# Kernel tuning notes

Measured on AMD Instinct MI355X. Metric: run time of the kernel, lower is better.

## Reference

```python
import jax, jax.numpy as jnp
import numpy as np

RADIUS = 0.2  # ball_query_radius
K = 64        # max_group_size


def _xavier(key, out_c, in_c):
    lim = float(np.sqrt(6.0 / (in_c + out_c)))
    return jax.random.uniform(key, (out_c, in_c), jnp.float32, -lim, lim)


def setup_inputs() -> dict:
    key = jax.random.key(0)
    ks = jax.random.split(key, 9)
    B, N, C_in, C_out = 8, 4096, 64, 256
    h = C_out // 2
    return {
        "points": jax.random.uniform(ks[0], (B, 3, N), jnp.float32),
        "point_features": jax.random.normal(ks[1], (B, C_in, N), jnp.float32),
        # point_point_net: Conv2d(3,C_in,1) -> ReLU -> Conv2d(C_in,C_in,1) -> ReLU -> Conv2d(C_in,h,1)
        "pw1": _xavier(ks[2], C_in, 3), "pb1": jnp.zeros(C_in, jnp.float32),
        "pw2": _xavier(ks[3], C_in, C_in), "pb2": jnp.zeros(C_in, jnp.float32),
        "pw3": _xavier(ks[4], h, C_in), "pb3": jnp.zeros(h, jnp.float32),
        # feature_point_net: Conv2d(C_in,C_in,1) -> ReLU -> Conv2d(C_in,C_in,1) -> ReLU -> Conv2d(C_in,h,1)
        "fw1": _xavier(ks[5], C_in, C_in), "fb1": jnp.zeros(C_in, jnp.float32),
        "fw2": _xavier(ks[6], C_in, C_in), "fb2": jnp.zeros(C_in, jnp.float32),
        "fw3": _xavier(ks[7], h, C_in), "fb3": jnp.zeros(h, jnp.float32),
    }


def _fps(pts, M):
    """Farthest point sampling: pts [N,3] -> M int32 indices (first pick = 0)."""
    N = pts.shape[0]

    def step(carry, _):
        mind, last = carry
        d = jnp.sum((pts - pts[last]) ** 2, axis=-1)
        mind = jnp.minimum(mind, d)
        nxt = jnp.argmax(mind).astype(jnp.int32)
        return (mind, nxt), last

    init = (jnp.full((N,), jnp.inf, pts.dtype), jnp.int32(0))
    _, idx = jax.lax.scan(step, init, None, length=M)
    return idx


def _ball_group(cent, pts):
    """cent [M,3], pts [N,3] -> first K in-radius neighbor indices [M,K] (padded with first hit)."""
    N = pts.shape[0]
    d2 = jnp.sum((cent[:, None, :] - pts[None, :, :]) ** 2, axis=-1)  # [M,N]
    score = jnp.where(d2 <= RADIUS * RADIUS, jnp.arange(N, dtype=jnp.int32), N)
    neg_top, _ = jax.lax.top_k(-score, K)     # K smallest scores = first K in-radius point ids
    sel = -neg_top                            # [M,K]
    sel = jnp.where(sel < N, sel, sel[:, :1]) # pad misses with first valid (centroid itself, dist 0)
    return sel


def _mlp3(x, w1, b1, w2, b2, w3, b3):
    """1x1 Conv2d stack applied along the channel axis; x [B,M,K,C]."""
    h = jax.nn.relu(jnp.einsum('bmkc,oc->bmko', x, w1) + b1)
    h = jax.nn.relu(jnp.einsum('bmkc,oc->bmko', h, w2) + b2)
    return jnp.einsum('bmkc,oc->bmko', h, w3) + b3


def reference(points, point_features, pw1, pb1, pw2, pb2, pw3, pb3,
              fw1, fb1, fw2, fb2, fw3, fb3):
    B, _, N = points.shape
    M = N // 4
    pts = points.transpose(0, 2, 1)            # [B,N,3]
    feats = point_features.transpose(0, 2, 1)  # [B,N,C]

    idx = jax.vmap(lambda p: _fps(p, M))(pts)                 # [B,M]
    cent = jnp.take_along_axis(pts, idx[:, :, None], axis=1)  # [B,M,3]
    sel = jax.vmap(_ball_group)(cent, pts)                    # [B,M,K]

    gpts = jax.vmap(lambda p, s: p[s])(pts, sel)              # [B,M,K,3]
    rel = gpts - cent[:, :, None, :]                          # local coords around centroid
    gfeat = jax.vmap(lambda f, s: f[s])(feats, sel)           # [B,M,K,C]

    p_out = jnp.max(_mlp3(rel, pw1, pb1, pw2, pb2, pw3, pb3), axis=2)    # [B,M,h]
    f_out = jnp.max(_mlp3(gfeat, fw1, fb1, fw2, fb2, fw3, fb3), axis=2)  # [B,M,h]

    centroid_features = jnp.concatenate([f_out, p_out], axis=-1).transpose(0, 2, 1)  # [B,C_out,M]
    centroids = cent.reshape(B, 3, M)  # replicates torch .view(B,3,-1) on the flat [B*M,3] buffer
    return centroids, centroid_features
```

## Files before the change

kernel.cpp:

```cpp
#include <hip/hip_runtime.h>
#include <hip/hip_bf16.h>

#define BB   8
#define NN   4096
#define MM   1024
#define KK   64
#define CIN  64
#define HH   128

#define R2F 0.039999999105930328f

static __device__ __forceinline__ float rnd_bf16(float v) {
    return __bfloat162float(__float2bfloat16(v));
}
static __device__ __forceinline__ unsigned int bf16bits(float v) {
    unsigned int u = __float_as_uint(v);
    return (u + 0x7FFFu + ((u >> 16) & 1u)) >> 16;
}

__global__ __launch_bounds__(256) void fps_featmlp_kernel(
    const float* __restrict__ pts,
    float* __restrict__ centf,
    float* __restrict__ outc,
    const float* __restrict__ feat,
    const float* __restrict__ fw1, const float* __restrict__ fb1,
    const float* __restrict__ fw2, const float* __restrict__ fb2,
    const float* __restrict__ fw3, const float* __restrict__ fb3,
    __hip_bfloat16* __restrict__ fout)
{
    __shared__ float smem[3 * NN];
    __shared__ unsigned long long akey[4];
    const int t = threadIdx.x;

    if (blockIdx.x < BB) {
        const int b = blockIdx.x;
        float* lx = smem;
        float* ly = smem + NN;
        float* lz = smem + 2 * NN;

        const float* px = pts + (size_t)b * 3 * NN;
        float x[16], y[16], z[16], mind[16];
#pragma unroll
        for (int i = 0; i < 16; ++i) {
            int p = t + i * 256;
            x[i] = px[p];
            y[i] = px[NN + p];
            z[i] = px[2 * NN + p];
            lx[p] = x[i]; ly[p] = y[i]; lz[p] = z[i];
            mind[i] = 3.4e38f;
        }
        if (t < 4) akey[t] = 0ULL;
        __syncthreads();

        float bx = lx[0], by = ly[0], bz = lz[0];

        for (int j = 0; j < MM; ++j) {
            if (t == 0) {
                int o = (b * MM + j) * 3;
                centf[o]    = bx; centf[o + 1] = by; centf[o + 2] = bz;
                outc[o]     = rnd_bf16(bx);
                outc[o + 1] = rnd_bf16(by);
                outc[o + 2] = rnd_bf16(bz);
                akey[(j + 2) & 3] = 0ULL;
            }
            float bd = -1.0f; int bi = 0;
#pragma unroll
            for (int i = 0; i < 16; ++i) {
                float dx = x[i] - bx, dy = y[i] - by, dz = z[i] - bz;
                float d = __fadd_rn(__fadd_rn(__fmul_rn(dx, dx), __fmul_rn(dy, dy)),
                                    __fmul_rn(dz, dz));
                float md = fminf(mind[i], d);
                mind[i] = md;
                if (md > bd) { bd = md; bi = t + i * 256; }
            }
            unsigned long long key =
                ((unsigned long long)__float_as_uint(bd) << 32) |
                (unsigned long long)(0xFFFFFFFFu - (unsigned)bi);
            atomicMax(&akey[j & 3], key);
            __syncthreads();
            unsigned long long bk = akey[j & 3];
            int best = (int)(0xFFFFFFFFu - (unsigned)(bk & 0xFFFFFFFFULL));
            bx = lx[best]; by = ly[best]; bz = lz[best];
        }
    } else {
        float* w1 = smem;
        float* w2 = smem + CIN * CIN;
        for (int i = t; i < CIN * CIN; i += 256) { w1[i] = fw1[i]; w2[i] = fw2[i]; }
        __syncthreads();

        const int gid = (blockIdx.x - BB) * 256 + t;
        const int b = gid >> 12, n = gid & (NN - 1);
        const float* fp = feat + (size_t)b * CIN * NN + n;

        float f[CIN];
#pragma unroll
        for (int c = 0; c < CIN; ++c) f[c] = fp[(size_t)c * NN];

        float h1[CIN];
        for (int o = 0; o < CIN; ++o) {
            float acc = fb1[o];
#pragma unroll
            for (int c = 0; c < CIN; ++c) acc = fmaf(f[c], w1[o * CIN + c], acc);
            h1[o] = fmaxf(acc, 0.f);
        }
        float h2[CIN];
        for (int o = 0; o < CIN; ++o) {
            float acc = fb2[o];
#pragma unroll
            for (int c = 0; c < CIN; ++c) acc = fmaf(h1[c], w2[o * CIN + c], acc);
            h2[o] = fmaxf(acc, 0.f);
        }
        __hip_bfloat16* op = fout + (size_t)gid * HH;
        for (int o = 0; o < HH; ++o) {
            float acc = fb3[o];
#pragma unroll
            for (int c = 0; c < CIN; ++c) acc = fmaf(h2[c], fw3[o * CIN + c], acc);
            op[o] = __float2bfloat16(acc);
        }
    }
}

#define H2SU 36
__global__ __launch_bounds__(64) void groupnet_kernel(
    const float* __restrict__ pts,
    const float* __restrict__ centf,
    const __hip_bfloat16* __restrict__ fout,
    const float* __restrict__ pw1, const float* __restrict__ pb1,
    const float* __restrict__ pw2, const float* __restrict__ pb2,
    const float* __restrict__ pw3, const float* __restrict__ pb3,
    float* __restrict__ outf)
{
    __shared__ unsigned int h2s[KK * H2SU];
    __shared__ int sels[KK];

    const int g = blockIdx.x;
    const int b = g >> 10, m = g & (MM - 1);
    const int lane = threadIdx.x;

    const float* pts_b = pts + (size_t)b * 3 * NN;
    const float cx = centf[(size_t)g * 3];
    const float cy = centf[(size_t)g * 3 + 1];
    const float cz = centf[(size_t)g * 3 + 2];

    int cnt = 0, first = 0;
    bool have_first = false;
    float fx[4], fy[4], fz[4];
#pragma unroll
    for (int q = 0; q < 4; ++q) {
        int p = q * 64 + lane;
        fx[q] = pts_b[p]; fy[q] = pts_b[NN + p]; fz[q] = pts_b[2 * NN + p];
    }
    for (int base = 0; base < NN; base += 256) {
#pragma unroll
        for (int q = 0; q < 4; ++q) {
            const int cb = base + q * 64;
            float vx = fx[q], vy = fy[q], vz = fz[q];
            const int pre = cb + 256 + lane;
            if (pre < NN) {
                fx[q] = pts_b[pre]; fy[q] = pts_b[NN + pre]; fz[q] = pts_b[2 * NN + pre];
            }
            float dx = vx - cx, dy = vy - cy, dz = vz - cz;
            float d2 = __fadd_rn(__fadd_rn(__fmul_rn(dx, dx), __fmul_rn(dy, dy)),
                                 __fmul_rn(dz, dz));
            bool in = (d2 <= R2F);
            unsigned long long mask = __ballot(in);
            if (!have_first && mask != 0ULL) {
                first = cb + (int)__builtin_ctzll(mask);
                have_first = true;
            }
            int pos = cnt + (int)__popcll(mask & ((1ULL << lane) - 1ULL));
            if (in && pos < KK) sels[pos] = cb + lane;
            cnt += (int)__popcll(mask);
        }
    }
    if (cnt < KK) {
        for (int q = cnt + lane; q < KK; q += 64) sels[q] = first;
    }
    __syncthreads();

    const int s = sels[lane];
    float* ob = outf + (size_t)b * 256 * MM + m;

    {
        const float x = pts_b[s]          - cx;
        const float y = pts_b[NN + s]     - cy;
        const float z = pts_b[2 * NN + s] - cz;
        float h1[CIN];
#pragma unroll
        for (int o = 0; o < CIN; ++o) {
            float acc = pb1[o];
            acc = fmaf(x, pw1[o * 3 + 0], acc);
            acc = fmaf(y, pw1[o * 3 + 1], acc);
            acc = fmaf(z, pw1[o * 3 + 2], acc);
            h1[o] = fmaxf(acc, 0.f);
        }
        for (int o8 = 0; o8 < CIN / 8; ++o8) {
            float a[8];
#pragma unroll
            for (int q = 0; q < 8; ++q) a[q] = pb2[o8 * 8 + q];
            for (int c = 0; c < CIN; ++c) {
                float hc = h1[c];
#pragma unroll
                for (int q = 0; q < 8; ++q)
                    a[q] = fmaf(hc, pw2[(o8 * 8 + q) * CIN + c], a[q]);
            }
            uint4 pk;
            pk.x = bf16bits(fmaxf(a[0], 0.f)) | (bf16bits(fmaxf(a[1], 0.f)) << 16);
            pk.y = bf16bits(fmaxf(a[2], 0.f)) | (bf16bits(fmaxf(a[3], 0.f)) << 16);
            pk.z = bf16bits(fmaxf(a[4], 0.f)) | (bf16bits(fmaxf(a[5], 0.f)) << 16);
            pk.w = bf16bits(fmaxf(a[6], 0.f)) | (bf16bits(fmaxf(a[7], 0.f)) << 16);
            *(uint4*)&h2s[lane * H2SU + o8 * 4] = pk;
        }
    }
    __syncthreads();

    {
        float w3a[CIN], w3b[CIN];
#pragma unroll
        for (int c = 0; c < CIN; ++c) {
            w3a[c] = pw3[(size_t)lane * CIN + c];
            w3b[c] = pw3[(size_t)(lane + 64) * CIN + c];
        }
        const float b3a = pb3[lane], b3b = pb3[lane + 64];
        float pa0 = -3.4e38f, pb0 = -3.4e38f;
        float pa1 = -3.4e38f, pb1v = -3.4e38f;
        for (int k = 0; k < KK / 2; ++k) {
            float va0 = b3a, vb0 = b3b, va1 = b3a, vb1 = b3b;
#pragma unroll
            for (int u4 = 0; u4 < 8; ++u4) {
                uint4 p0 = *(const uint4*)&h2s[k * H2SU + u4 * 4];
                uint4 p1 = *(const uint4*)&h2s[(k + 32) * H2SU + u4 * 4];
                const unsigned int* w0 = &p0.x;
                const unsigned int* w1 = &p1.x;
#pragma unroll
                for (int j = 0; j < 4; ++j) {
                    int c = u4 * 8 + j * 2;
                    float h0lo = __uint_as_float(w0[j] << 16);
                    float h0hi = __uint_as_float(w0[j] & 0xFFFF0000u);
                    float h1lo = __uint_as_float(w1[j] << 16);
                    float h1hi = __uint_as_float(w1[j] & 0xFFFF0000u);
                    va0 = fmaf(h0lo, w3a[c],     va0); vb0 = fmaf(h0lo, w3b[c],     vb0);
                    va1 = fmaf(h1lo, w3a[c],     va1); vb1 = fmaf(h1lo, w3b[c],     vb1);
                    va0 = fmaf(h0hi, w3a[c + 1], va0); vb0 = fmaf(h0hi, w3b[c + 1], vb0);
                    va1 = fmaf(h1hi, w3a[c + 1], va1); vb1 = fmaf(h1hi, w3b[c + 1], vb1);
                }
            }
            pa0 = fmaxf(pa0, va0); pb0  = fmaxf(pb0,  vb0);
            pa1 = fmaxf(pa1, va1); pb1v = fmaxf(pb1v, vb1);
        }
        ob[(size_t)(128 + lane) * MM] = rnd_bf16(fmaxf(pa0, pa1));
        ob[(size_t)(192 + lane) * MM] = rnd_bf16(fmaxf(pb0, pb1v));
    }

    {
        const __hip_bfloat16* fb_ = fout + (size_t)b * NN * HH;
        unsigned int pf[4];
#pragma unroll
        for (int q = 0; q < 4; ++q)
            pf[q] = ((const unsigned int*)(fb_ + (size_t)sels[q] * HH))[lane];
        float alo[4], ahi[4];
#pragma unroll
        for (int q = 0; q < 4; ++q) { alo[q] = -3.4e38f; ahi[q] = -3.4e38f; }
        for (int k = 0; k < KK; k += 4) {
#pragma unroll
            for (int q = 0; q < 4; ++q) {
                unsigned int w = pf[q];
                int nk = k + 4 + q;
                if (nk < KK)
                    pf[q] = ((const unsigned int*)(fb_ + (size_t)sels[nk] * HH))[lane];
                alo[q] = fmaxf(alo[q], __uint_as_float(w << 16));
                ahi[q] = fmaxf(ahi[q], __uint_as_float(w & 0xFFFF0000u));
            }
        }
        float lo = fmaxf(fmaxf(alo[0], alo[1]), fmaxf(alo[2], alo[3]));
        float hi = fmaxf(fmaxf(ahi[0], ahi[1]), fmaxf(ahi[2], ahi[3]));
        ob[(size_t)(2 * lane) * MM]     = lo;
        ob[(size_t)(2 * lane + 1) * MM] = hi;
    }
}

extern "C" void kernel_launch(void* const* d_in, const int* in_sizes, int n_in,
                              void* d_out, int out_size, void* d_ws, size_t ws_size,
                              hipStream_t stream) {
    const float* pts  = (const float*)d_in[0];
    const float* feat = (const float*)d_in[1];
    const float* pw1  = (const float*)d_in[2];
    const float* pb1  = (const float*)d_in[3];
    const float* pw2  = (const float*)d_in[4];
    const float* pb2  = (const float*)d_in[5];
    const float* pw3  = (const float*)d_in[6];
    const float* pb3  = (const float*)d_in[7];
    const float* fw1  = (const float*)d_in[8];
    const float* fb1  = (const float*)d_in[9];
    const float* fw2  = (const float*)d_in[10];
    const float* fb2  = (const float*)d_in[11];
    const float* fw3  = (const float*)d_in[12];
    const float* fb3  = (const float*)d_in[13];

    float* out = (float*)d_out;

    float* centf = (float*)d_ws;
    __hip_bfloat16* fout = (__hip_bfloat16*)((char*)d_ws + (size_t)BB * MM * 3 * 4);

    fps_featmlp_kernel<<<BB + (BB * NN) / 256, 256, 0, stream>>>(
        pts, centf, out, feat, fw1, fb1, fw2, fb2, fw3, fb3, fout);
    groupnet_kernel<<<BB * MM, 64, 0, stream>>>(
        pts, centf, fout,
        pw1, pb1, pw2, pb2, pw3, pb3,
        out + (size_t)BB * MM * 3);
}
```

Measured before the change: 971.3 us.

## Split group MLP across four waves, DPP wave reduction in FPS argmax

```diff
diff --git a/kernel.cpp b/kernel.cpp
--- a/kernel.cpp
+++ b/kernel.cpp
@@ -16,6 +16,25 @@
 static __device__ __forceinline__ unsigned int bf16bits(float v) {
     unsigned int u = __float_as_uint(v);
     return (u + 0x7FFFu + ((u >> 16) & 1u)) >> 16;
+}
+
+static __device__ __forceinline__ void wave_max_key(unsigned int& hi,
+                                                    unsigned int& lo) {
+#define DPP_STEP(ctrl)                                                        \
+    {                                                                         \
+        unsigned int h2 = (unsigned int)__builtin_amdgcn_update_dpp(          \
+            0, (int)hi, (ctrl), 0xF, 0xF, true);                              \
+        unsigned int l2 = (unsigned int)__builtin_amdgcn_update_dpp(          \
+            0, (int)lo, (ctrl), 0xF, 0xF, true);                              \
+        if (h2 > hi || (h2 == hi && l2 > lo)) { hi = h2; lo = l2; }           \
+    }
+    DPP_STEP(0x111)
+    DPP_STEP(0x112)
+    DPP_STEP(0x114)
+    DPP_STEP(0x118)
+    DPP_STEP(0x142)
+    DPP_STEP(0x143)
+#undef DPP_STEP
 }
 
 __global__ __launch_bounds__(256) void fps_featmlp_kernel(
@@ -26,7 +45,9 @@
     const float* __restrict__ fw1, const float* __restrict__ fb1,
     const float* __restrict__ fw2, const float* __restrict__ fb2,
     const float* __restrict__ fw3, const float* __restrict__ fb3,
-    __hip_bfloat16* __restrict__ fout)
+    __hip_bfloat16* __restrict__ fout,
+    const float* __restrict__ pw3,
+    float* __restrict__ pw3T)
 {
     __shared__ float smem[3 * NN];
     __shared__ unsigned long long akey[4];
@@ -73,16 +94,18 @@
                 mind[i] = md;
                 if (md > bd) { bd = md; bi = t + i * 256; }
             }
-            unsigned long long key =
-                ((unsigned long long)__float_as_uint(bd) << 32) |
-                (unsigned long long)(0xFFFFFFFFu - (unsigned)bi);
-            atomicMax(&akey[j & 3], key);
+            unsigned int khi = __float_as_uint(bd);
+            unsigned int klo = 0xFFFFFFFFu - (unsigned)bi;
+            wave_max_key(khi, klo);
+            if ((t & 63) == 63)
+                atomicMax(&akey[j & 3],
+                          ((unsigned long long)khi << 32) | (unsigned long long)klo);
             __syncthreads();
             unsigned long long bk = akey[j & 3];
             int best = (int)(0xFFFFFFFFu - (unsigned)(bk & 0xFFFFFFFFULL));
             bx = lx[best]; by = ly[best]; bz = lz[best];
         }
-    } else {
+    } else if (blockIdx.x < BB + (BB * NN) / 256) {
         float* w1 = smem;
         float* w2 = smem + CIN * CIN;
         for (int i = t; i < CIN * CIN; i += 256) { w1[i] = fw1[i]; w2[i] = fw2[i]; }
@@ -117,71 +140,80 @@
             for (int c = 0; c < CIN; ++c) acc = fmaf(h2[c], fw3[o * CIN + c], acc);
             op[o] = __float2bfloat16(acc);
         }
+    } else {
+        for (int i = t; i < HH * CIN; i += 256) {
+            int o = i >> 6, c = i & 63;
+            pw3T[c * HH + o] = pw3[i];
+        }
     }
 }
 
 #define H2SU 36
-__global__ __launch_bounds__(64) void groupnet_kernel(
+__global__ __launch_bounds__(256, 4) void groupnet_kernel(
     const float* __restrict__ pts,
     const float* __restrict__ centf,
     const __hip_bfloat16* __restrict__ fout,
     const float* __restrict__ pw1, const float* __restrict__ pb1,
     const float* __restrict__ pw2, const float* __restrict__ pb2,
-    const float* __restrict__ pw3, const float* __restrict__ pb3,
+    const float* __restrict__ pw3T, const float* __restrict__ pb3,
     float* __restrict__ outf)
 {
     __shared__ unsigned int h2s[KK * H2SU];
     __shared__ int sels[KK];
+    __shared__ float part[4][4][64];
 
     const int g = blockIdx.x;
     const int b = g >> 10, m = g & (MM - 1);
-    const int lane = threadIdx.x;
+    const int t = threadIdx.x;
+    const int w = t >> 6, lane = t & 63;
 
     const float* pts_b = pts + (size_t)b * 3 * NN;
     const float cx = centf[(size_t)g * 3];
     const float cy = centf[(size_t)g * 3 + 1];
     const float cz = centf[(size_t)g * 3 + 2];
 
-    int cnt = 0, first = 0;
-    bool have_first = false;
-    float fx[4], fy[4], fz[4];
-#pragma unroll
-    for (int q = 0; q < 4; ++q) {
-        int p = q * 64 + lane;
-        fx[q] = pts_b[p]; fy[q] = pts_b[NN + p]; fz[q] = pts_b[2 * NN + p];
-    }
-    for (int base = 0; base < NN; base += 256) {
+    if (w == 0) {
+        int cnt = 0, first = 0;
+        bool have_first = false;
+        float fx[4], fy[4], fz[4];
 #pragma unroll
         for (int q = 0; q < 4; ++q) {
-            const int cb = base + q * 64;
-            float vx = fx[q], vy = fy[q], vz = fz[q];
-            const int pre = cb + 256 + lane;
-            if (pre < NN) {
-                fx[q] = pts_b[pre]; fy[q] = pts_b[NN + pre]; fz[q] = pts_b[2 * NN + pre];
-            }
-            float dx = vx - cx, dy = vy - cy, dz = vz - cz;
-            float d2 = __fadd_rn(__fadd_rn(__fmul_rn(dx, dx), __fmul_rn(dy, dy)),
-                                 __fmul_rn(dz, dz));
-            bool in = (d2 <= R2F);
-            unsigned long long mask = __ballot(in);
-            if (!have_first && mask != 0ULL) {
-                first = cb + (int)__builtin_ctzll(mask);
-                have_first = true;
-            }
-            int pos = cnt + (int)__popcll(mask & ((1ULL << lane) - 1ULL));
-            if (in && pos < KK) sels[pos] = cb + lane;
-            cnt += (int)__popcll(mask);
-        }
-    }
-    if (cnt < KK) {
-        for (int q = cnt + lane; q < KK; q += 64) sels[q] = first;
+            int p = q * 64 + lane;
+            fx[q] = pts_b[p]; fy[q] = pts_b[NN + p]; fz[q] = pts_b[2 * NN + p];
+        }
+        for (int base = 0; base < NN; base += 256) {
+#pragma unroll
+            for (int q = 0; q < 4; ++q) {
+                const int cb = base + q * 64;
+                float vx = fx[q], vy = fy[q], vz = fz[q];
+                const int pre = cb + 256 + lane;
+                if (pre < NN) {
+                    fx[q] = pts_b[pre]; fy[q] = pts_b[NN + pre]; fz[q] = pts_b[2 * NN + pre];
+                }
+                float dx = vx - cx, dy = vy - cy, dz = vz - cz;
+                float d2 = __fadd_rn(__fadd_rn(__fmul_rn(dx, dx), __fmul_rn(dy, dy)),
+                                     __fmul_rn(dz, dz));
+                bool in = (d2 <= R2F);
+                unsigned long long mask = __ballot(in);
+                if (!have_first && mask != 0ULL) {
+                    first = cb + (int)__builtin_ctzll(mask);
+                    have_first = true;
+                }
+                int pos = cnt + (int)__popcll(mask & ((1ULL << lane) - 1ULL));
+                if (in && pos < KK) sels[pos] = cb + lane;
+                cnt += (int)__popcll(mask);
+            }
+        }
+        if (cnt < KK) {
+            for (int q = cnt + lane; q < KK; q += 64) sels[q] = first;
+        }
     }
     __syncthreads();
 
-    const int s = sels[lane];
     float* ob = outf + (size_t)b * 256 * MM + m;
 
     {
+        const int s = sels[lane];
         const float x = pts_b[s]          - cx;
         const float y = pts_b[NN + s]     - cy;
         const float z = pts_b[2 * NN + s] - cz;
@@ -194,88 +226,85 @@
             acc = fmaf(z, pw1[o * 3 + 2], acc);
             h1[o] = fmaxf(acc, 0.f);
         }
-        for (int o8 = 0; o8 < CIN / 8; ++o8) {
+        for (int o8 = 0; o8 < 2; ++o8) {
+            const int ob0 = w * 16 + o8 * 8;
             float a[8];
 #pragma unroll
-            for (int q = 0; q < 8; ++q) a[q] = pb2[o8 * 8 + q];
+            for (int q = 0; q < 8; ++q) a[q] = pb2[ob0 + q];
             for (int c = 0; c < CIN; ++c) {
                 float hc = h1[c];
 #pragma unroll
                 for (int q = 0; q < 8; ++q)
-                    a[q] = fmaf(hc, pw2[(o8 * 8 + q) * CIN + c], a[q]);
+                    a[q] = fmaf(hc, pw2[(ob0 + q) * CIN + c], a[q]);
             }
             uint4 pk;
             pk.x = bf16bits(fmaxf(a[0], 0.f)) | (bf16bits(fmaxf(a[1], 0.f)) << 16);
             pk.y = bf16bits(fmaxf(a[2], 0.f)) | (bf16bits(fmaxf(a[3], 0.f)) << 16);
             pk.z = bf16bits(fmaxf(a[4], 0.f)) | (bf16bits(fmaxf(a[5], 0.f)) << 16);
             pk.w = bf16bits(fmaxf(a[6], 0.f)) | (bf16bits(fmaxf(a[7], 0.f)) << 16);
-            *(uint4*)&h2s[lane * H2SU + o8 * 4] = pk;
+            *(uint4*)&h2s[lane * H2SU + w * 8 + o8 * 4] = pk;
         }
     }
     __syncthreads();
 
     {
-        float w3a[CIN], w3b[CIN];
-#pragma unroll
-        for (int c = 0; c < CIN; ++c) {
-            w3a[c] = pw3[(size_t)lane * CIN + c];
-            w3b[c] = pw3[(size_t)(lane + 64) * CIN + c];
-        }
-        const float b3a = pb3[lane], b3b = pb3[lane + 64];
-        float pa0 = -3.4e38f, pb0 = -3.4e38f;
-        float pa1 = -3.4e38f, pb1v = -3.4e38f;
-        for (int k = 0; k < KK / 2; ++k) {
-            float va0 = b3a, vb0 = b3b, va1 = b3a, vb1 = b3b;
-#pragma unroll
-            for (int u4 = 0; u4 < 8; ++u4) {
-                uint4 p0 = *(const uint4*)&h2s[k * H2SU + u4 * 4];
-                uint4 p1 = *(const uint4*)&h2s[(k + 32) * H2SU + u4 * 4];
-                const unsigned int* w0 = &p0.x;
-                const unsigned int* w1 = &p1.x;
-#pragma unroll
-                for (int j = 0; j < 4; ++j) {
-                    int c = u4 * 8 + j * 2;
-                    float h0lo = __uint_as_float(w0[j] << 16);
-                    float h0hi = __uint_as_float(w0[j] & 0xFFFF0000u);
-                    float h1lo = __uint_as_float(w1[j] << 16);
-                    float h1hi = __uint_as_float(w1[j] & 0xFFFF0000u);
-                    va0 = fmaf(h0lo, w3a[c],     va0); vb0 = fmaf(h0lo, w3b[c],     vb0);
-                    va1 = fmaf(h1lo, w3a[c],     va1); vb1 = fmaf(h1lo, w3b[c],     vb1);
-                    va0 = fmaf(h0hi, w3a[c + 1], va0); vb0 = fmaf(h0hi, w3b[c + 1], vb0);
-                    va1 = fmaf(h1hi, w3a[c + 1], va1); vb1 = fmaf(h1hi, w3b[c + 1], vb1);
+        const int k0 = w * 16;
+        float wv[CIN];
+#pragma unroll 2
+        for (int half = 0; half < 2; ++half) {
+            const int ch = half * 64 + lane;
+#pragma unroll
+            for (int c = 0; c < CIN; ++c) wv[c] = pw3T[c * HH + ch];
+            const float bias = pb3[ch];
+            float p0 = -3.4e38f, p1 = -3.4e38f;
+            for (int kk = 0; kk < 8; ++kk) {
+                float v0 = bias, v1 = bias;
+#pragma unroll
+                for (int u4 = 0; u4 < 8; ++u4) {
+                    uint4 q0 = *(const uint4*)&h2s[(k0 + kk) * H2SU + u4 * 4];
+                    uint4 q1 = *(const uint4*)&h2s[(k0 + 8 + kk) * H2SU + u4 * 4];
+                    const unsigned int* a0 = &q0.x;
+                    const unsigned int* a1 = &q1.x;
+#pragma unroll
+                    for (int jj = 0; jj < 4; ++jj) {
+                        int c = u4 * 8 + jj * 2;
+                        v0 = fmaf(__uint_as_float(a0[jj] << 16),         wv[c],     v0);
+                        v0 = fmaf(__uint_as_float(a0[jj] & 0xFFFF0000u), wv[c + 1], v0);
+                        v1 = fmaf(__uint_as_float(a1[jj] << 16),         wv[c],     v1);
+                        v1 = fmaf(__uint_as_float(a1[jj] & 0xFFFF0000u), wv[c + 1], v1);
+                    }
                 }
-            }
-            pa0 = fmaxf(pa0, va0); pb0  = fmaxf(pb0,  vb0);
-            pa1 = fmaxf(pa1, va1); pb1v = fmaxf(pb1v, vb1);
-        }
-        ob[(size_t)(128 + lane) * MM] = rnd_bf16(fmaxf(pa0, pa1));
-        ob[(size_t)(192 + lane) * MM] = rnd_bf16(fmaxf(pb0, pb1v));
+                p0 = fmaxf(p0, v0); p1 = fmaxf(p1, v1);
+            }
+            part[w][half][lane] = fmaxf(p0, p1);
+        }
     }
 
     {
         const __hip_bfloat16* fb_ = fout + (size_t)b * NN * HH;
-        unsigned int pf[4];
-#pragma unroll
-        for (int q = 0; q < 4; ++q)
-            pf[q] = ((const unsigned int*)(fb_ + (size_t)sels[q] * HH))[lane];
-        float alo[4], ahi[4];
-#pragma unroll
-        for (int q = 0; q < 4; ++q) { alo[q] = -3.4e38f; ahi[q] = -3.4e38f; }
-        for (int k = 0; k < KK; k += 4) {
-#pragma unroll
-            for (int q = 0; q < 4; ++q) {
-                unsigned int w = pf[q];
-                int nk = k + 4 + q;
-                if (nk < KK)
-                    pf[q] = ((const unsigned int*)(fb_ + (size_t)sels[nk] * HH))[lane];
-                alo[q] = fmaxf(alo[q], __uint_as_float(w << 16));
-                ahi[q] = fmaxf(ahi[q], __uint_as_float(w & 0xFFFF0000u));
-            }
-        }
-        float lo = fmaxf(fmaxf(alo[0], alo[1]), fmaxf(alo[2], alo[3]));
-        float hi = fmaxf(fmaxf(ahi[0], ahi[1]), fmaxf(ahi[2], ahi[3]));
-        ob[(size_t)(2 * lane) * MM]     = lo;
-        ob[(size_t)(2 * lane + 1) * MM] = hi;
+        const int k0 = w * 16;
+        float l0 = -3.4e38f, h0 = -3.4e38f, l1 = -3.4e38f, h1v = -3.4e38f;
+        for (int kk = 0; kk < 8; ++kk) {
+            unsigned int u0 = ((const unsigned int*)(fb_ + (size_t)sels[k0 + kk]     * HH))[lane];
+            unsigned int u1 = ((const unsigned int*)(fb_ + (size_t)sels[k0 + 8 + kk] * HH))[lane];
+            l0  = fmaxf(l0,  __uint_as_float(u0 << 16));
+            h0  = fmaxf(h0,  __uint_as_float(u0 & 0xFFFF0000u));
+            l1  = fmaxf(l1,  __uint_as_float(u1 << 16));
+            h1v = fmaxf(h1v, __uint_as_float(u1 & 0xFFFF0000u));
+        }
+        part[w][2][lane] = fmaxf(l0, l1);
+        part[w][3][lane] = fmaxf(h0, h1v);
+    }
+    __syncthreads();
+
+    {
+        const int slot = (w == 0) ? 2 : (w == 1) ? 3 : (w == 2) ? 0 : 1;
+        float v = fmaxf(fmaxf(part[0][slot][lane], part[1][slot][lane]),
+                        fmaxf(part[2][slot][lane], part[3][slot][lane]));
+        if      (w == 0) ob[(size_t)(2 * lane)     * MM] = v;
+        else if (w == 1) ob[(size_t)(2 * lane + 1) * MM] = v;
+        else if (w == 2) ob[(size_t)(128 + lane)   * MM] = rnd_bf16(v);
+        else             ob[(size_t)(192 + lane)   * MM] = rnd_bf16(v);
     }
 }
 
@@ -301,11 +330,13 @@
 
     float* centf = (float*)d_ws;
     __hip_bfloat16* fout = (__hip_bfloat16*)((char*)d_ws + (size_t)BB * MM * 3 * 4);
-
-    fps_featmlp_kernel<<<BB + (BB * NN) / 256, 256, 0, stream>>>(
-        pts, centf, out, feat, fw1, fb1, fw2, fb2, fw3, fb3, fout);
-    groupnet_kernel<<<BB * MM, 64, 0, stream>>>(
+    float* pw3T = (float*)((char*)d_ws + (size_t)BB * MM * 3 * 4
+                           + (size_t)BB * NN * HH * 2);
+
+    fps_featmlp_kernel<<<BB + (BB * NN) / 256 + 1, 256, 0, stream>>>(
+        pts, centf, out, feat, fw1, fb1, fw2, fb2, fw3, fb3, fout, pw3, pw3T);
+    groupnet_kernel<<<BB * MM, 256, 0, stream>>>(
         pts, centf, fout,
-        pw1, pb1, pw2, pb2, pw3, pb3,
+        pw1, pb1, pw2, pb2, pw3T, pb3,
         out + (size_t)BB * MM * 3);
 }
```

New measurement: 1.356 ms. 39.6% more time.

## Fuse FPS and grouping into one persistent kernel with flag-based producer-consumer overlap

Applied to the files above, without the earlier changes.

```diff
diff --git a/kernel.cpp b/kernel.cpp
--- a/kernel.cpp
+++ b/kernel.cpp
@@ -10,6 +10,9 @@
 
 #define R2F 0.039999999105930328f
 
+#define NPROD (BB + (BB * NN) / 256)
+#define H2SU  36
+
 static __device__ __forceinline__ float rnd_bf16(float v) {
     return __bfloat162float(__float2bfloat16(v));
 }
@@ -17,8 +20,13 @@
     unsigned int u = __float_as_uint(v);
     return (u + 0x7FFFu + ((u >> 16) & 1u)) >> 16;
 }
-
-__global__ __launch_bounds__(256) void fps_featmlp_kernel(
+static __device__ __forceinline__ void wavefence() {
+    __builtin_amdgcn_wave_barrier();
+    __threadfence_block();
+    __builtin_amdgcn_wave_barrier();
+}
+
+__global__ __launch_bounds__(256, 3) void fused_kernel(
     const float* __restrict__ pts,
     float* __restrict__ centf,
     float* __restrict__ outc,
@@ -26,7 +34,12 @@
     const float* __restrict__ fw1, const float* __restrict__ fb1,
     const float* __restrict__ fw2, const float* __restrict__ fb2,
     const float* __restrict__ fw3, const float* __restrict__ fb3,
-    __hip_bfloat16* __restrict__ fout)
+    __hip_bfloat16* __restrict__ fout,
+    const float* __restrict__ pw1, const float* __restrict__ pb1,
+    const float* __restrict__ pw2, const float* __restrict__ pb2,
+    const float* __restrict__ pw3, const float* __restrict__ pb3,
+    float* __restrict__ outf,
+    unsigned int* __restrict__ flags)
 {
     __shared__ float smem[3 * NN];
     __shared__ unsigned long long akey[4];
@@ -61,6 +74,9 @@
                 outc[o]     = rnd_bf16(bx);
                 outc[o + 1] = rnd_bf16(by);
                 outc[o + 2] = rnd_bf16(bz);
+                if ((j & 15) == 15)
+                    __hip_atomic_store(&flags[b], (unsigned int)(j + 1),
+                                       __ATOMIC_RELEASE, __HIP_MEMORY_SCOPE_AGENT);
                 akey[(j + 2) & 3] = 0ULL;
             }
             float bd = -1.0f; int bi = 0;
@@ -82,7 +98,7 @@
             int best = (int)(0xFFFFFFFFu - (unsigned)(bk & 0xFFFFFFFFULL));
             bx = lx[best]; by = ly[best]; bz = lz[best];
         }
-    } else {
+    } else if (blockIdx.x < NPROD) {
         float* w1 = smem;
         float* w2 = smem + CIN * CIN;
         for (int i = t; i < CIN * CIN; i += 256) { w1[i] = fw1[i]; w2[i] = fw2[i]; }
@@ -117,165 +133,170 @@
             for (int c = 0; c < CIN; ++c) acc = fmaf(h2[c], fw3[o * CIN + c], acc);
             op[o] = __float2bfloat16(acc);
         }
-    }
-}
-
-#define H2SU 36
-__global__ __launch_bounds__(64) void groupnet_kernel(
-    const float* __restrict__ pts,
-    const float* __restrict__ centf,
-    const __hip_bfloat16* __restrict__ fout,
-    const float* __restrict__ pw1, const float* __restrict__ pb1,
-    const float* __restrict__ pw2, const float* __restrict__ pb2,
-    const float* __restrict__ pw3, const float* __restrict__ pb3,
-    float* __restrict__ outf)
-{
-    __shared__ unsigned int h2s[KK * H2SU];
-    __shared__ int sels[KK];
-
-    const int g = blockIdx.x;
-    const int b = g >> 10, m = g & (MM - 1);
-    const int lane = threadIdx.x;
-
-    const float* pts_b = pts + (size_t)b * 3 * NN;
-    const float cx = centf[(size_t)g * 3];
-    const float cy = centf[(size_t)g * 3 + 1];
-    const float cz = centf[(size_t)g * 3 + 2];
-
-    int cnt = 0, first = 0;
-    bool have_first = false;
-    float fx[4], fy[4], fz[4];
-#pragma unroll
-    for (int q = 0; q < 4; ++q) {
-        int p = q * 64 + lane;
-        fx[q] = pts_b[p]; fy[q] = pts_b[NN + p]; fz[q] = pts_b[2 * NN + p];
-    }
-    for (int base = 0; base < NN; base += 256) {
+        __threadfence();
+        __syncthreads();
+        if (t == 0)
+            __hip_atomic_fetch_add(&flags[8], 1u,
+                                   __ATOMIC_RELEASE, __HIP_MEMORY_SCOPE_AGENT);
+    } else {
+        const int wv = t >> 6, lane = t & 63;
+        unsigned int* h2w = ((unsigned int*)smem) + wv * (KK * H2SU);
+        int* selw = ((int*)smem) + 4 * (KK * H2SU) + wv * KK;
+
+        const int g = (blockIdx.x - NPROD) * 4 + wv;
+        const int b = g >> 10, m = g & (MM - 1);
+
+        while (__hip_atomic_load(&flags[b], __ATOMIC_RELAXED,
+                                 __HIP_MEMORY_SCOPE_AGENT) <= (unsigned)m)
+            __builtin_amdgcn_s_sleep(8);
+        (void)__hip_atomic_load(&flags[b], __ATOMIC_ACQUIRE,
+                                __HIP_MEMORY_SCOPE_AGENT);
+
+        const float* pts_b = pts + (size_t)b * 3 * NN;
+        const float cx = centf[(size_t)g * 3];
+        const float cy = centf[(size_t)g * 3 + 1];
+        const float cz = centf[(size_t)g * 3 + 2];
+
+        int cnt = 0, first = 0;
+        bool have_first = false;
+        float fx[4], fy[4], fz[4];
 #pragma unroll
         for (int q = 0; q < 4; ++q) {
-            const int cb = base + q * 64;
-            float vx = fx[q], vy = fy[q], vz = fz[q];
-            const int pre = cb + 256 + lane;
-            if (pre < NN) {
-                fx[q] = pts_b[pre]; fy[q] = pts_b[NN + pre]; fz[q] = pts_b[2 * NN + pre];
-            }
-            float dx = vx - cx, dy = vy - cy, dz = vz - cz;
-            float d2 = __fadd_rn(__fadd_rn(__fmul_rn(dx, dx), __fmul_rn(dy, dy)),
-                                 __fmul_rn(dz, dz));
-            bool in = (d2 <= R2F);
-            unsigned long long mask = __ballot(in);
-            if (!have_first && mask != 0ULL) {
-                first = cb + (int)__builtin_ctzll(mask);
-                have_first = true;
-            }
-            int pos = cnt + (int)__popcll(mask & ((1ULL << lane) - 1ULL));
-            if (in && pos < KK) sels[pos] = cb + lane;
-            cnt += (int)__popcll(mask);
-        }
-    }
-    if (cnt < KK) {
-        for (int q = cnt + lane; q < KK; q += 64) sels[q] = first;
-    }
-    __syncthreads();
-
-    const int s = sels[lane];
-    float* ob = outf + (size_t)b * 256 * MM + m;
-
-    {
-        const float x = pts_b[s]          - cx;
-        const float y = pts_b[NN + s]     - cy;
-        const float z = pts_b[2 * NN + s] - cz;
-        float h1[CIN];
-#pragma unroll
-        for (int o = 0; o < CIN; ++o) {
-            float acc = pb1[o];
-            acc = fmaf(x, pw1[o * 3 + 0], acc);
-            acc = fmaf(y, pw1[o * 3 + 1], acc);
-            acc = fmaf(z, pw1[o * 3 + 2], acc);
-            h1[o] = fmaxf(acc, 0.f);
-        }
-        for (int o8 = 0; o8 < CIN / 8; ++o8) {
-            float a[8];
-#pragma unroll
-            for (int q = 0; q < 8; ++q) a[q] = pb2[o8 * 8 + q];
+            int p = q * 64 + lane;
+            fx[q] = pts_b[p]; fy[q] = pts_b[NN + p]; fz[q] = pts_b[2 * NN + p];
+        }
+        for (int base = 0; base < NN; base += 256) {
+#pragma unroll
+            for (int q = 0; q < 4; ++q) {
+                const int cb = base + q * 64;
+                float vx = fx[q], vy = fy[q], vz = fz[q];
+                const int pre = cb + 256 + lane;
+                if (pre < NN) {
+                    fx[q] = pts_b[pre]; fy[q] = pts_b[NN + pre]; fz[q] = pts_b[2 * NN + pre];
+                }
+                float dx = vx - cx, dy = vy - cy, dz = vz - cz;
+                float d2 = __fadd_rn(__fadd_rn(__fmul_rn(dx, dx), __fmul_rn(dy, dy)),
+                                     __fmul_rn(dz, dz));
+                bool in = (d2 <= R2F);
+                unsigned long long mask = __ballot(in);
+                if (!have_first && mask != 0ULL) {
+                    first = cb + (int)__builtin_ctzll(mask);
+                    have_first = true;
+                }
+                int pos = cnt + (int)__popcll(mask & ((1ULL << lane) - 1ULL));
+                if (in && pos < KK) selw[pos] = cb + lane;
+                cnt += (int)__popcll(mask);
+            }
+        }
+        if (cnt < KK) {
+            for (int q = cnt + lane; q < KK; q += 64) selw[q] = first;
+        }
+        wavefence();
+
+        const int s = selw[lane];
+        float* ob = outf + (size_t)b * 256 * MM + m;
+
+        {
+            const float x = pts_b[s]          - cx;
+            const float y = pts_b[NN + s]     - cy;
+            const float z = pts_b[2 * NN + s] - cz;
+            float h1[CIN];
+#pragma unroll
+            for (int o = 0; o < CIN; ++o) {
+                float acc = pb1[o];
+                acc = fmaf(x, pw1[o * 3 + 0], acc);
+                acc = fmaf(y, pw1[o * 3 + 1], acc);
+                acc = fmaf(z, pw1[o * 3 + 2], acc);
+                h1[o] = fmaxf(acc, 0.f);
+            }
+            for (int o8 = 0; o8 < CIN / 8; ++o8) {
+                float a[8];
+#pragma unroll
+                for (int q = 0; q < 8; ++q) a[q] = pb2[o8 * 8 + q];
+                for (int c = 0; c < CIN; ++c) {
+                    float hc = h1[c];
+#pragma unroll
+                    for (int q = 0; q < 8; ++q)
+                        a[q] = fmaf(hc, pw2[(o8 * 8 + q) * CIN + c], a[q]);
+                }
+                uint4 pk;
+                pk.x = bf16bits(fmaxf(a[0], 0.f)) | (bf16bits(fmaxf(a[1], 0.f)) << 16);
+                pk.y = bf16bits(fmaxf(a[2], 0.f)) | (bf16bits(fmaxf(a[3], 0.f)) << 16);
+                pk.z = bf16bits(fmaxf(a[4], 0.f)) | (bf16bits(fmaxf(a[5], 0.f)) << 16);
+                pk.w = bf16bits(fmaxf(a[6], 0.f)) | (bf16bits(fmaxf(a[7], 0.f)) << 16);
+                *(uint4*)&h2w[lane * H2SU + o8 * 4] = pk;
+            }
+        }
+        wavefence();
+
+        {
+            float w3a[CIN], w3b[CIN];
+#pragma unroll
             for (int c = 0; c < CIN; ++c) {
-                float hc = h1[c];
-#pragma unroll
-                for (int q = 0; q < 8; ++q)
-                    a[q] = fmaf(hc, pw2[(o8 * 8 + q) * CIN + c], a[q]);
-            }
-            uint4 pk;
-            pk.x = bf16bits(fmaxf(a[0], 0.f)) | (bf16bits(fmaxf(a[1], 0.f)) << 16);
-            pk.y = bf16bits(fmaxf(a[2], 0.f)) | (bf16bits(fmaxf(a[3], 0.f)) << 16);
-            pk.z = bf16bits(fmaxf(a[4], 0.f)) | (bf16bits(fmaxf(a[5], 0.f)) << 16);
-            pk.w = bf16bits(fmaxf(a[6], 0.f)) | (bf16bits(fmaxf(a[7], 0.f)) << 16);
-            *(uint4*)&h2s[lane * H2SU + o8 * 4] = pk;
-        }
-    }
-    __syncthreads();
-
-    {
-        float w3a[CIN], w3b[CIN];
-#pragma unroll
-        for (int c = 0; c < CIN; ++c) {
-            w3a[c] = pw3[(size_t)lane * CIN + c];
-            w3b[c] = pw3[(size_t)(lane + 64) * CIN + c];
-        }
-        const float b3a = pb3[lane], b3b = pb3[lane + 64];
-        float pa0 = -3.4e38f, pb0 = -3.4e38f;
-        float pa1 = -3.4e38f, pb1v = -3.4e38f;
-        for (int k = 0; k < KK / 2; ++k) {
-            float va0 = b3a, vb0 = b3b, va1 = b3a, vb1 = b3b;
-#pragma unroll
-            for (int u4 = 0; u4 < 8; ++u4) {
-                uint4 p0 = *(const uint4*)&h2s[k * H2SU + u4 * 4];
-                uint4 p1 = *(const uint4*)&h2s[(k + 32) * H2SU + u4 * 4];
-                const unsigned int* w0 = &p0.x;
-                const unsigned int* w1 = &p1.x;
-#pragma unroll
-                for (int j = 0; j < 4; ++j) {
-                    int c = u4 * 8 + j * 2;
-                    float h0lo = __uint_as_float(w0[j] << 16);
-                    float h0hi = __uint_as_float(w0[j] & 0xFFFF0000u);
-                    float h1lo = __uint_as_float(w1[j] << 16);
-                    float h1hi = __uint_as_float(w1[j] & 0xFFFF0000u);
-                    va0 = fmaf(h0lo, w3a[c],     va0); vb0 = fmaf(h0lo, w3b[c],     vb0);
-                    va1 = fmaf(h1lo, w3a[c],     va1); vb1 = fmaf(h1lo, w3b[c],     vb1);
-                    va0 = fmaf(h0hi, w3a[c + 1], va0); vb0 = fmaf(h0hi, w3b[c + 1], vb0);
-                    va1 = fmaf(h1hi, w3a[c + 1], va1); vb1 = fmaf(h1hi, w3b[c + 1], vb1);
-                }
-            }
-            pa0 = fmaxf(pa0, va0); pb0  = fmaxf(pb0,  vb0);
-            pa1 = fmaxf(pa1, va1); pb1v = fmaxf(pb1v, vb1);
-        }
-        ob[(size_t)(128 + lane) * MM] = rnd_bf16(fmaxf(pa0, pa1));
-        ob[(size_t)(192 + lane) * MM] = rnd_bf16(fmaxf(pb0, pb1v));
-    }
-
-    {
-        const __hip_bfloat16* fb_ = fout + (size_t)b * NN * HH;
-        unsigned int pf[4];
-#pragma unroll
-        for (int q = 0; q < 4; ++q)
-            pf[q] = ((const unsigned int*)(fb_ + (size_t)sels[q] * HH))[lane];
-        float alo[4], ahi[4];
-#pragma unroll
-        for (int q = 0; q < 4; ++q) { alo[q] = -3.4e38f; ahi[q] = -3.4e38f; }
-        for (int k = 0; k < KK; k += 4) {
-#pragma unroll
-            for (int q = 0; q < 4; ++q) {
-                unsigned int w = pf[q];
-                int nk = k + 4 + q;
-                if (nk < KK)
-                    pf[q] = ((const unsigned int*)(fb_ + (size_t)sels[nk] * HH))[lane];
-                alo[q] = fmaxf(alo[q], __uint_as_float(w << 16));
-                ahi[q] = fmaxf(ahi[q], __uint_as_float(w & 0xFFFF0000u));
-            }
-        }
-        float lo = fmaxf(fmaxf(alo[0], alo[1]), fmaxf(alo[2], alo[3]));
-        float hi = fmaxf(fmaxf(ahi[0], ahi[1]), fmaxf(ahi[2], ahi[3]));
-        ob[(size_t)(2 * lane) * MM]     = lo;
-        ob[(size_t)(2 * lane + 1) * MM] = hi;
+                w3a[c] = pw3[(size_t)lane * CIN + c];
+                w3b[c] = pw3[(size_t)(lane + 64) * CIN + c];
+            }
+            const float b3a = pb3[lane], b3b = pb3[lane + 64];
+            float pa0 = -3.4e38f, pb0 = -3.4e38f;
+            float pa1 = -3.4e38f, pb1v = -3.4e38f;
+            for (int k = 0; k < KK / 2; ++k) {
+                float va0 = b3a, vb0 = b3b, va1 = b3a, vb1 = b3b;
+#pragma unroll
+                for (int u4 = 0; u4 < 8; ++u4) {
+                    uint4 p0 = *(const uint4*)&h2w[k * H2SU + u4 * 4];
+                    uint4 p1 = *(const uint4*)&h2w[(k + 32) * H2SU + u4 * 4];
+                    const unsigned int* w0 = &p0.x;
+                    const unsigned int* w1 = &p1.x;
+#pragma unroll
+                    for (int jj = 0; jj < 4; ++jj) {
+                        int c = u4 * 8 + jj * 2;
+                        float h0lo = __uint_as_float(w0[jj] << 16);
+                        float h0hi = __uint_as_float(w0[jj] & 0xFFFF0000u);
+                        float h1lo = __uint_as_float(w1[jj] << 16);
+                        float h1hi = __uint_as_float(w1[jj] & 0xFFFF0000u);
+                        va0 = fmaf(h0lo, w3a[c],     va0); vb0 = fmaf(h0lo, w3b[c],     vb0);
+                        va1 = fmaf(h1lo, w3a[c],     va1); vb1 = fmaf(h1lo, w3b[c],     vb1);
+                        va0 = fmaf(h0hi, w3a[c + 1], va0); vb0 = fmaf(h0hi, w3b[c + 1], vb0);
+                        va1 = fmaf(h1hi, w3a[c + 1], va1); vb1 = fmaf(h1hi, w3b[c + 1], vb1);
+                    }
+                }
+                pa0 = fmaxf(pa0, va0); pb0  = fmaxf(pb0,  vb0);
+                pa1 = fmaxf(pa1, va1); pb1v = fmaxf(pb1v, vb1);
+            }
+            ob[(size_t)(128 + lane) * MM] = rnd_bf16(fmaxf(pa0, pa1));
+            ob[(size_t)(192 + lane) * MM] = rnd_bf16(fmaxf(pb0, pb1v));
+        }
+
+        while (__hip_atomic_load(&flags[8], __ATOMIC_RELAXED,
+                                 __HIP_MEMORY_SCOPE_AGENT) < (unsigned)(NPROD - BB))
+            __builtin_amdgcn_s_sleep(8);
+        (void)__hip_atomic_load(&flags[8], __ATOMIC_ACQUIRE,
+                                __HIP_MEMORY_SCOPE_AGENT);
+        {
+            const __hip_bfloat16* fb_ = fout + (size_t)b * NN * HH;
+            unsigned int pf[4];
+#pragma unroll
+            for (int q = 0; q < 4; ++q)
+                pf[q] = ((const unsigned int*)(fb_ + (size_t)selw[q] * HH))[lane];
+            float alo[4], ahi[4];
+#pragma unroll
+            for (int q = 0; q < 4; ++q) { alo[q] = -3.4e38f; ahi[q] = -3.4e38f; }
+            for (int k = 0; k < KK; k += 4) {
+#pragma unroll
+                for (int q = 0; q < 4; ++q) {
+                    unsigned int wversion = pf[q];
+                    int nk = k + 4 + q;
+                    if (nk < KK)
+                        pf[q] = ((const unsigned int*)(fb_ + (size_t)selw[nk] * HH))[lane];
+                    alo[q] = fmaxf(alo[q], __uint_as_float(wversion << 16));
+                    ahi[q] = fmaxf(ahi[q], __uint_as_float(wversion & 0xFFFF0000u));
+                }
+            }
+            float lo = fmaxf(fmaxf(alo[0], alo[1]), fmaxf(alo[2], alo[3]));
+            float hi = fmaxf(fmaxf(ahi[0], ahi[1]), fmaxf(ahi[2], ahi[3]));
+            ob[(size_t)(2 * lane) * MM]     = lo;
+            ob[(size_t)(2 * lane + 1) * MM] = hi;
+        }
     }
 }
 
@@ -301,11 +322,13 @@
 
     float* centf = (float*)d_ws;
     __hip_bfloat16* fout = (__hip_bfloat16*)((char*)d_ws + (size_t)BB * MM * 3 * 4);
-
-    fps_featmlp_kernel<<<BB + (BB * NN) / 256, 256, 0, stream>>>(
-        pts, centf, out, feat, fw1, fb1, fw2, fb2, fw3, fb3, fout);
-    groupnet_kernel<<<BB * MM, 64, 0, stream>>>(
-        pts, centf, fout,
+    unsigned int* flags = (unsigned int*)((char*)d_ws + (size_t)BB * MM * 3 * 4
+                                          + (size_t)BB * NN * HH * 2);
+
+    hipMemsetAsync(flags, 0, 64, stream);
+
+    fused_kernel<<<NPROD + (BB * MM) / 4, 256, 0, stream>>>(
+        pts, centf, out, feat, fw1, fb1, fw2, fb2, fw3, fb3, fout,
         pw1, pb1, pw2, pb2, pw3, pb3,
-        out + (size_t)BB * MM * 3);
-}
+        out + (size_t)BB * MM * 3, flags);
+}
```

Result: faster. 848.3 us (-12.7%).
